# Optimization experiments

Measured on AMD Instinct MI355X. Metric: run time of the kernel, lower is better.

Reference implementation:

```python
import jax, jax.numpy as jnp
import numpy as np

N_IMG, C_IN, H, W = 8, 8, 136, 200
N_INST = 512
CHANNELS = 8
STRIDE = 8
MASK_OUT_STRIDE = 4
# sizes_of_interest + [last*2], per __init__
SOI = jnp.asarray([64.0, 128.0, 256.0, 512.0, 1024.0, 2048.0], dtype=jnp.float32)
W_NUMS = [(C_IN + 2) * CHANNELS, CHANNELS * CHANNELS, CHANNELS]
B_NUMS = [CHANNELS, CHANNELS, 1]
N_PARAMS = sum(W_NUMS) + sum(B_NUMS)  # 169


def compute_locations(h, w, stride):
    # matches adet compute_locations: centers of stride-sized cells, (x, y)
    shifts_x = jnp.arange(w, dtype=jnp.float32) * stride + stride // 2
    shifts_y = jnp.arange(h, dtype=jnp.float32) * stride + stride // 2
    ys, xs = jnp.meshgrid(shifts_y, shifts_x, indexing='ij')
    return jnp.stack([xs.reshape(-1), ys.reshape(-1)], axis=1)  # [h*w, 2]


def bilinear_up_align_corners(x, out_h, out_w):
    # x: [n, h, w]; F.interpolate(mode='bilinear', align_corners=True)
    n, h, w = x.shape
    ys = jnp.linspace(0.0, h - 1.0, out_h)
    xs = jnp.linspace(0.0, w - 1.0, out_w)
    y0 = jnp.floor(ys).astype(jnp.int32)
    x0 = jnp.floor(xs).astype(jnp.int32)
    y1 = jnp.minimum(y0 + 1, h - 1)
    x1 = jnp.minimum(x0 + 1, w - 1)
    wy = (ys - y0.astype(jnp.float32))[None, :, None]
    wx = (xs - x0.astype(jnp.float32))[None, None, :]
    top = x[:, y0, :]
    bot = x[:, y1, :]
    row0 = top[:, :, x0] * (1.0 - wx) + top[:, :, x1] * wx
    row1 = bot[:, :, x0] * (1.0 - wx) + bot[:, :, x1] * wx
    return row0 * (1.0 - wy) + row1 * wy


def dice_coefficient(x, target):
    eps = 1e-5
    n = x.shape[0]
    x = x.reshape(n, -1)
    target = target.reshape(n, -1)
    intersection = jnp.sum(x * target, axis=1)
    union = jnp.sum(x * x, axis=1) + jnp.sum(target * target, axis=1) + eps
    return 1.0 - 2.0 * intersection / union


def setup_inputs() -> dict:
    key = jax.random.key(0)
    ks = jax.random.split(key, 6)
    mask_feats = jax.random.normal(ks[0], (N_IMG, C_IN, H, W), jnp.float32)
    mask_head_params = jax.random.normal(ks[1], (N_INST, N_PARAMS), jnp.float32) * 0.1
    instance_locations = jax.random.uniform(ks[2], (N_INST, 2), jnp.float32) * jnp.asarray(
        [W * STRIDE, H * STRIDE], dtype=jnp.float32)
    gt_masks = (jax.random.uniform(ks[3], (N_INST, 2 * H, 2 * W), jnp.float32) > 0.5).astype(jnp.float32)
    im_inds = jax.random.randint(ks[4], (N_INST,), 0, N_IMG, jnp.int32)
    fpn_levels = jax.random.randint(ks[5], (N_INST,), 0, 5, jnp.int32)
    return {
        'mask_feats': mask_feats,
        'mask_head_params': mask_head_params,
        'instance_locations': instance_locations,
        'gt_masks': gt_masks,
        'im_inds': im_inds,
        'fpn_levels': fpn_levels,
        'mask_feat_stride': 8,
    }


def reference(mask_feats, mask_head_params, instance_locations, gt_masks, im_inds, fpn_levels, mask_feat_stride):
    n_inst = mask_head_params.shape[0]
    # relative coordinates: instance center minus every grid location, / size-of-interest
    locations = compute_locations(H, W, mask_feat_stride)          # [H*W, 2]
    rel = instance_locations[:, None, :] - locations[None, :, :]   # [n, H*W, 2]
    rel = jnp.transpose(rel, (0, 2, 1)) / SOI[fpn_levels][:, None, None]
    rel = rel.reshape(n_inst, 2, H, W)
    feats = mask_feats[im_inds]                                    # gather [n, C_IN, H, W]
    x = jnp.concatenate([rel, feats], axis=1)                      # [n, C_IN+2, H, W]

    # parse_dynamic_params: split per-instance params into 1x1 conv weights/biases
    splits = np.cumsum(W_NUMS + B_NUMS)[:-1].tolist()
    p = jnp.split(mask_head_params, splits, axis=1)
    w0 = p[0].reshape(n_inst, CHANNELS, C_IN + 2)
    w1 = p[1].reshape(n_inst, CHANNELS, CHANNELS)
    w2 = p[2].reshape(n_inst, 1, CHANNELS)
    b0, b1, b2 = p[3], p[4], p[5]

    # grouped 1x1 convs (groups = n_inst) == per-instance channel GEMM
    x = jax.nn.relu(jnp.einsum('nchw,noc->nohw', x, w0) + b0[:, :, None, None])
    x = jax.nn.relu(jnp.einsum('nchw,noc->nohw', x, w1) + b1[:, :, None, None])
    logits = jnp.einsum('nchw,noc->nohw', x, w2) + b2[:, :, None, None]  # [n, 1, H, W]

    up = mask_feat_stride // MASK_OUT_STRIDE
    logits_up = bilinear_up_align_corners(logits[:, 0], H * up, W * up)
    scores = jax.nn.sigmoid(logits_up)
    loss = dice_coefficient(scores, gt_masks)                      # [n]
    return loss
```

## Files before the change

### kernel.cpp

```cpp
#include <hip/hip_runtime.h>
#include <math.h>

#define NIMG 8
#define CIN 8
#define Hh 136
#define Ww 200
#define HW (Hh * Ww)
#define OH 272
#define OW 400
#define NINST 512
#define NPAR 169
#define TROWS 34
#define NTILES 8
#define LROWS 19
#define PART_BYTES ((size_t)NINST * NTILES * 3 * 4)

#define PINV(x) asm volatile("" : "+v"(x))
#define PINS(x) asm volatile("" : "+s"(x))
#define MEMFENCE asm volatile("" ::: "memory")
#define SCHEDBAR __builtin_amdgcn_sched_barrier(0)

__device__ __forceinline__ void mlp_tile_reg(
    float* __restrict__ slog, const float* __restrict__ fb0,
    const float* __restrict__ pp, int ly0, int lycnt, int tid,
    const float (&A0)[8], const float (&Ax)[8], const float (&Ay)[8])
{
    const int tpx = lycnt * Ww;
    const float* fbase = fb0 + ly0 * Ww;

    for (int px = tid * 2; px < tpx; px += 512) {
        MEMFENCE;
        float Wf[64];
#pragma unroll
        for (int o = 0; o < 8; o++)
#pragma unroll
            for (int c = 0; c < 8; c++) Wf[o * 8 + c] = pp[o * 10 + 2 + c];
#pragma unroll
        for (int i = 0; i < 64; i++) PINS(Wf[i]);

        const int yy = px / 200;
        const int x  = px - yy * 200;
        const float yf = (float)(ly0 + yy);
        const float* fb = fbase + px;
        float f[8][2];
#pragma unroll
        for (int c = 0; c < 8; c++) {
            const float2 t = *reinterpret_cast<const float2*>(fb + c * HW);
            f[c][0] = t.x; f[c][1] = t.y;
        }
        float h[8][2];
#pragma unroll
        for (int o = 0; o < 8; o++) {
            const float pre = A0[o] + Ay[o] * yf;
#pragma unroll
            for (int p = 0; p < 2; p++) {
                const float xf = (float)(x + p);
                float a = pre + Ax[o] * xf;
#pragma unroll
                for (int c = 0; c < 8; c++) a += Wf[o * 8 + c] * f[c][p];
                h[o][p] = fmaxf(a, 0.0f);
            }
        }
#pragma unroll
        for (int o = 0; o < 8; o++) { PINV(h[o][0]); PINV(h[o][1]); }
        SCHEDBAR;

        MEMFENCE;
        float w1[64];
#pragma unroll
        for (int k = 0; k < 64; k++) w1[k] = pp[80 + k];
#pragma unroll
        for (int k = 0; k < 64; k++) PINS(w1[k]);
        float w2[8], b1[8], b2;
#pragma unroll
        for (int k = 0; k < 8; k++) { w2[k] = pp[144 + k]; b1[k] = pp[160 + k]; }
        b2 = pp[168];
#pragma unroll
        for (int k = 0; k < 8; k++) { PINV(w2[k]); PINV(b1[k]); }
        PINV(b2);

        float o2[2];
#pragma unroll
        for (int p = 0; p < 2; p++) {
            float g[8];
#pragma unroll
            for (int o = 0; o < 8; o++) {
                float a = b1[o];
#pragma unroll
                for (int c = 0; c < 8; c++) a += w1[o * 8 + c] * h[c][p];
                g[o] = fmaxf(a, 0.0f);
            }
            float lg = b2;
#pragma unroll
            for (int c = 0; c < 8; c++) lg += w2[c] * g[c];
            o2[p] = lg;
        }
        *reinterpret_cast<float2*>(&slog[px]) = make_float2(o2[0], o2[1]);
        SCHEDBAR;
    }
}

__device__ __forceinline__ void dice_tile(
    const float* __restrict__ slog, const float* __restrict__ gtn,
    int oy0, int ly0, int lycnt, int tid,
    float& aI, float& aS, float& aT)
{
    const float sy = 135.0f / 271.0f;
    const float sx = 199.0f / 399.0f;
    for (int g4 = tid; g4 < TROWS * (OW / 4); g4 += 256) {
        const int ry = g4 / 100;
        const int gx = (g4 - ry * 100) * 4;
        const int oy = oy0 + ry;
        const float ysf = (float)oy * sy;
        const int y0 = (int)ysf;
        const float wy = ysf - (float)y0;
        const int y1 = (y0 + 1 > Hh - 1) ? (Hh - 1) : (y0 + 1);
        int r0i = y0 - ly0, r1i = y1 - ly0;
        r0i = r0i < 0 ? 0 : (r0i > lycnt - 1 ? lycnt - 1 : r0i);
        r1i = r1i < 0 ? 0 : (r1i > lycnt - 1 ? lycnt - 1 : r1i);
        const float* s0 = &slog[r0i * Ww];
        const float* s1 = &slog[r1i * Ww];

        const float4 t4 = *reinterpret_cast<const float4*>(gtn + ry * OW + gx);
        const float tv[4] = { t4.x, t4.y, t4.z, t4.w };
#pragma unroll
        for (int p = 0; p < 4; p++) {
            const int ox = gx + p;
            const float xsf = (float)ox * sx;
            const int x0 = (int)xsf;
            const float wx = xsf - (float)x0;
            const int x1 = (x0 + 1 > Ww - 1) ? (Ww - 1) : (x0 + 1);
            const float v00 = s0[x0];
            const float v01 = s0[x1];
            const float v10 = s1[x0];
            const float v11 = s1[x1];
            const float top = v00 + wx * (v01 - v00);
            const float bot = v10 + wx * (v11 - v10);
            const float v   = top + wy * (bot - top);
            const float s   = __fdividef(1.0f, 1.0f + __expf(-v));
            aI += s * tv[p];
            aS += s * s;
            aT += tv[p];
        }
    }
}

#define LOAD_AFFINE                                                             \
    const float ix = iloc[2 * n + 0];                                           \
    const float iy = iloc[2 * n + 1];                                           \
    const int   im = iminds[n];                                                 \
    const float invsoi = 1.0f / (float)(64 << lvls[n]);                         \
    const float* pp = pars + n * NPAR;                                          \
    float A0[8], Ax[8], Ay[8];                                                  \
    _Pragma("unroll")                                                           \
    for (int o = 0; o < 8; o++) {                                               \
        const float wx0 = pp[o * 10 + 0];                                       \
        const float wy0 = pp[o * 10 + 1];                                       \
        Ax[o] = -8.0f * invsoi * wx0;                                           \
        Ay[o] = -8.0f * invsoi * wy0;                                           \
        A0[o] = pp[152 + o] + (wx0 * (ix - 4.0f) + wy0 * (iy - 4.0f)) * invsoi; \
    }                                                                           \
    _Pragma("unroll")                                                           \
    for (int o = 0; o < 8; o++) { PINV(A0[o]); PINV(Ax[o]); PINV(Ay[o]); }

__global__ __launch_bounds__(256, 6) void dmh_tile(
    const float* __restrict__ feats,
    const float* __restrict__ pars,
    const float* __restrict__ iloc,
    const float* __restrict__ gt,
    const int* __restrict__ iminds,
    const int* __restrict__ lvls,
    float* __restrict__ part)
{
    __shared__ float slog[LROWS * Ww];
    __shared__ float sred[12];

    const int n    = blockIdx.y;
    const int tile = blockIdx.x;
    const int tid  = threadIdx.x;

    LOAD_AFFINE

    const float sy = 135.0f / 271.0f;
    const int oy0 = tile * TROWS;
    const int ly0 = (int)((float)oy0 * sy);
    int lyL = (int)((float)(oy0 + TROWS - 1) * sy) + 1;
    if (lyL > Hh - 1) lyL = Hh - 1;
    const int lycnt = lyL - ly0 + 1;

    const float* fb0 = feats + (size_t)im * (CIN * HW);
    mlp_tile_reg(slog, fb0, pp, ly0, lycnt, tid, A0, Ax, Ay);
    __syncthreads();

    float aI = 0.0f, aS = 0.0f, aT = 0.0f;
    const float* gtn = gt + (size_t)n * (OH * OW) + (size_t)oy0 * OW;
    dice_tile(slog, gtn, oy0, ly0, lycnt, tid, aI, aS, aT);

#pragma unroll
    for (int off = 32; off > 0; off >>= 1) {
        aI += __shfl_down(aI, off, 64);
        aS += __shfl_down(aS, off, 64);
        aT += __shfl_down(aT, off, 64);
    }
    const int wv = tid >> 6;
    if ((tid & 63) == 0) {
        sred[wv * 3 + 0] = aI;
        sred[wv * 3 + 1] = aS;
        sred[wv * 3 + 2] = aT;
    }
    __syncthreads();
    if (tid == 0) {
        float* pt = part + (size_t)(n * NTILES + tile) * 3;
        pt[0] = sred[0] + sred[3] + sred[6] + sred[9];
        pt[1] = sred[1] + sred[4] + sred[7] + sred[10];
        pt[2] = sred[2] + sred[5] + sred[8] + sred[11];
    }
}

__global__ __launch_bounds__(256) void dmh_fin2(const float* __restrict__ part,
                                                float* __restrict__ out)
{
    const int i = blockIdx.x * 256 + threadIdx.x;
    if (i < NINST) {
        float I = 0.0f, S = 0.0f, T = 0.0f;
#pragma unroll
        for (int t = 0; t < NTILES; t++) {
            const float* pt = part + (size_t)(i * NTILES + t) * 3;
            I += pt[0]; S += pt[1]; T += pt[2];
        }
        out[i] = 1.0f - 2.0f * I / (S + T + 1e-5f);
    }
}

__global__ __launch_bounds__(256, 6) void dmh_one(
    const float* __restrict__ feats,
    const float* __restrict__ pars,
    const float* __restrict__ iloc,
    const float* __restrict__ gt,
    const int* __restrict__ iminds,
    const int* __restrict__ lvls,
    float* __restrict__ out)
{
    __shared__ float slog[LROWS * Ww];
    __shared__ float sred[12];

    const int n   = blockIdx.x;
    const int tid = threadIdx.x;

    LOAD_AFFINE

    const float sy = 135.0f / 271.0f;
    const float* fb0 = feats + (size_t)im * (CIN * HW);

    float aI = 0.0f, aS = 0.0f, aT = 0.0f;
    for (int tile = 0; tile < NTILES; tile++) {
        const int oy0 = tile * TROWS;
        const int ly0 = (int)((float)oy0 * sy);
        int lyL = (int)((float)(oy0 + TROWS - 1) * sy) + 1;
        if (lyL > Hh - 1) lyL = Hh - 1;
        const int lycnt = lyL - ly0 + 1;

        mlp_tile_reg(slog, fb0, pp, ly0, lycnt, tid, A0, Ax, Ay);
        __syncthreads();
        const float* gtn = gt + (size_t)n * (OH * OW) + (size_t)oy0 * OW;
        dice_tile(slog, gtn, oy0, ly0, lycnt, tid, aI, aS, aT);
        __syncthreads();
    }

#pragma unroll
    for (int off = 32; off > 0; off >>= 1) {
        aI += __shfl_down(aI, off, 64);
        aS += __shfl_down(aS, off, 64);
        aT += __shfl_down(aT, off, 64);
    }
    const int wv = tid >> 6;
    if ((tid & 63) == 0) {
        sred[wv * 3 + 0] = aI;
        sred[wv * 3 + 1] = aS;
        sred[wv * 3 + 2] = aT;
    }
    __syncthreads();
    if (tid == 0) {
        const float I = sred[0] + sred[3] + sred[6] + sred[9];
        const float S = sred[1] + sred[4] + sred[7] + sred[10];
        const float T = sred[2] + sred[5] + sred[8] + sred[11];
        out[n] = 1.0f - 2.0f * I / (S + T + 1e-5f);
    }
}

extern "C" void kernel_launch(void* const* d_in, const int* in_sizes, int n_in,
                              void* d_out, int out_size, void* d_ws, size_t ws_size,
                              hipStream_t stream) {
    const float* feats  = (const float*)d_in[0];
    const float* pars   = (const float*)d_in[1];
    const float* iloc   = (const float*)d_in[2];
    const float* gt     = (const float*)d_in[3];
    const int*   iminds = (const int*)d_in[4];
    const int*   lvls   = (const int*)d_in[5];

    if (ws_size >= PART_BYTES) {
        float* part = (float*)d_ws;
        dim3 g(NTILES, NINST);
        dmh_tile<<<g, 256, 0, stream>>>(feats, pars, iloc, gt, iminds, lvls, part);
        dmh_fin2<<<(NINST + 255) / 256, 256, 0, stream>>>(part, (float*)d_out);
    } else {
        dmh_one<<<NINST, 256, 0, stream>>>(feats, pars, iloc, gt, iminds, lvls,
                                           (float*)d_out);
    }
}
```

Before: 394.6 us.

## Warp-specialize MLP into layer0 producer and layer1/2 consumer via double-buffered LDS

The tile kernel now splits its 256 threads into two groups. Threads 0-127 load features and compute the first 1x1 conv layer into a double-buffered shared strip of hidden activations, while threads 128-255 apply the second and third layers to the previous strip. The goal is to overlap global feature loads with the later layers and keep each group's weights in registers without reloading them every iteration. The cost is extra shared memory (32 KB) and a barrier per strip, and the occupancy hint drops from 6 to 3 blocks.

```diff
diff --git a/kernel.cpp b/kernel.cpp
--- a/kernel.cpp
+++ b/kernel.cpp
@@ -13,92 +13,13 @@
 #define TROWS 34
 #define NTILES 8
 #define LROWS 19
+#define SPX 512
 #define PART_BYTES ((size_t)NINST * NTILES * 3 * 4)
 
 #define PINV(x) asm volatile("" : "+v"(x))
 #define PINS(x) asm volatile("" : "+s"(x))
 #define MEMFENCE asm volatile("" ::: "memory")
 #define SCHEDBAR __builtin_amdgcn_sched_barrier(0)
-
-__device__ __forceinline__ void mlp_tile_reg(
-    float* __restrict__ slog, const float* __restrict__ fb0,
-    const float* __restrict__ pp, int ly0, int lycnt, int tid,
-    const float (&A0)[8], const float (&Ax)[8], const float (&Ay)[8])
-{
-    const int tpx = lycnt * Ww;
-    const float* fbase = fb0 + ly0 * Ww;
-
-    for (int px = tid * 2; px < tpx; px += 512) {
-        MEMFENCE;
-        float Wf[64];
-#pragma unroll
-        for (int o = 0; o < 8; o++)
-#pragma unroll
-            for (int c = 0; c < 8; c++) Wf[o * 8 + c] = pp[o * 10 + 2 + c];
-#pragma unroll
-        for (int i = 0; i < 64; i++) PINS(Wf[i]);
-
-        const int yy = px / 200;
-        const int x  = px - yy * 200;
-        const float yf = (float)(ly0 + yy);
-        const float* fb = fbase + px;
-        float f[8][2];
-#pragma unroll
-        for (int c = 0; c < 8; c++) {
-            const float2 t = *reinterpret_cast<const float2*>(fb + c * HW);
-            f[c][0] = t.x; f[c][1] = t.y;
-        }
-        float h[8][2];
-#pragma unroll
-        for (int o = 0; o < 8; o++) {
-            const float pre = A0[o] + Ay[o] * yf;
-#pragma unroll
-            for (int p = 0; p < 2; p++) {
-                const float xf = (float)(x + p);
-                float a = pre + Ax[o] * xf;
-#pragma unroll
-                for (int c = 0; c < 8; c++) a += Wf[o * 8 + c] * f[c][p];
-                h[o][p] = fmaxf(a, 0.0f);
-            }
-        }
-#pragma unroll
-        for (int o = 0; o < 8; o++) { PINV(h[o][0]); PINV(h[o][1]); }
-        SCHEDBAR;
-
-        MEMFENCE;
-        float w1[64];
-#pragma unroll
-        for (int k = 0; k < 64; k++) w1[k] = pp[80 + k];
-#pragma unroll
-        for (int k = 0; k < 64; k++) PINS(w1[k]);
-        float w2[8], b1[8], b2;
-#pragma unroll
-        for (int k = 0; k < 8; k++) { w2[k] = pp[144 + k]; b1[k] = pp[160 + k]; }
-        b2 = pp[168];
-#pragma unroll
-        for (int k = 0; k < 8; k++) { PINV(w2[k]); PINV(b1[k]); }
-        PINV(b2);
-
-        float o2[2];
-#pragma unroll
-        for (int p = 0; p < 2; p++) {
-            float g[8];
-#pragma unroll
-            for (int o = 0; o < 8; o++) {
-                float a = b1[o];
-#pragma unroll
-                for (int c = 0; c < 8; c++) a += w1[o * 8 + c] * h[c][p];
-                g[o] = fmaxf(a, 0.0f);
-            }
-            float lg = b2;
-#pragma unroll
-            for (int c = 0; c < 8; c++) lg += w2[c] * g[c];
-            o2[p] = lg;
-        }
-        *reinterpret_cast<float2*>(&slog[px]) = make_float2(o2[0], o2[1]);
-        SCHEDBAR;
-    }
-}
 
 __device__ __forceinline__ void dice_tile(
     const float* __restrict__ slog, const float* __restrict__ gtn,
@@ -145,25 +66,7 @@
     }
 }
 
-#define LOAD_AFFINE                                                             \
-    const float ix = iloc[2 * n + 0];                                           \
-    const float iy = iloc[2 * n + 1];                                           \
-    const int   im = iminds[n];                                                 \
-    const float invsoi = 1.0f / (float)(64 << lvls[n]);                         \
-    const float* pp = pars + n * NPAR;                                          \
-    float A0[8], Ax[8], Ay[8];                                                  \
-    _Pragma("unroll")                                                           \
-    for (int o = 0; o < 8; o++) {                                               \
-        const float wx0 = pp[o * 10 + 0];                                       \
-        const float wy0 = pp[o * 10 + 1];                                       \
-        Ax[o] = -8.0f * invsoi * wx0;                                           \
-        Ay[o] = -8.0f * invsoi * wy0;                                           \
-        A0[o] = pp[152 + o] + (wx0 * (ix - 4.0f) + wy0 * (iy - 4.0f)) * invsoi; \
-    }                                                                           \
-    _Pragma("unroll")                                                           \
-    for (int o = 0; o < 8; o++) { PINV(A0[o]); PINV(Ax[o]); PINV(Ay[o]); }
-
-__global__ __launch_bounds__(256, 6) void dmh_tile(
+__global__ __launch_bounds__(256, 3) void dmh_tile(
     const float* __restrict__ feats,
     const float* __restrict__ pars,
     const float* __restrict__ iloc,
@@ -173,13 +76,12 @@
     float* __restrict__ part)
 {
     __shared__ float slog[LROWS * Ww];
+    __shared__ float hbuf[2][8][SPX];
     __shared__ float sred[12];
 
     const int n    = blockIdx.y;
     const int tile = blockIdx.x;
     const int tid  = threadIdx.x;
-
-    LOAD_AFFINE
 
     const float sy = 135.0f / 271.0f;
     const int oy0 = tile * TROWS;
@@ -187,10 +89,120 @@
     int lyL = (int)((float)(oy0 + TROWS - 1) * sy) + 1;
     if (lyL > Hh - 1) lyL = Hh - 1;
     const int lycnt = lyL - ly0 + 1;
-
-    const float* fb0 = feats + (size_t)im * (CIN * HW);
-    mlp_tile_reg(slog, fb0, pp, ly0, lycnt, tid, A0, Ax, Ay);
-    __syncthreads();
+    const int tpx = lycnt * Ww;
+    const int nstrips = (tpx + SPX - 1) / SPX;
+
+    const float* pp = pars + n * NPAR;
+
+    if (tid < 128) {
+        const float ix = iloc[2 * n + 0];
+        const float iy = iloc[2 * n + 1];
+        const int   im = iminds[n];
+        const float invsoi = 1.0f / (float)(64 << lvls[n]);
+        float Wf[64], A0[8], Ax[8], Ay[8];
+#pragma unroll
+        for (int o = 0; o < 8; o++) {
+            const float wx0 = pp[o * 10 + 0];
+            const float wy0 = pp[o * 10 + 1];
+            Ax[o] = -8.0f * invsoi * wx0;
+            Ay[o] = -8.0f * invsoi * wy0;
+            A0[o] = pp[152 + o] + (wx0 * (ix - 4.0f) + wy0 * (iy - 4.0f)) * invsoi;
+#pragma unroll
+            for (int c = 0; c < 8; c++) Wf[o * 8 + c] = pp[o * 10 + 2 + c];
+        }
+#pragma unroll
+        for (int i = 0; i < 64; i++) PINS(Wf[i]);
+#pragma unroll
+        for (int o = 0; o < 8; o++) { PINV(A0[o]); PINV(Ax[o]); PINV(Ay[o]); }
+
+        const float* fbase = feats + (size_t)im * (CIN * HW) + ly0 * Ww;
+
+        for (int k = 0; k < nstrips + 1; ++k) {
+            if (k < nstrips) {
+                const int base = k * SPX + tid * 4;
+                if (base < tpx) {
+                    const int yy = base / 200;
+                    const int x  = base - yy * 200;
+                    const float yf = (float)(ly0 + yy);
+                    const float* fb = fbase + base;
+                    float f[8][4];
+#pragma unroll
+                    for (int c = 0; c < 8; c++) {
+                        const float4 t = *reinterpret_cast<const float4*>(fb + c * HW);
+                        f[c][0] = t.x; f[c][1] = t.y; f[c][2] = t.z; f[c][3] = t.w;
+                    }
+#pragma unroll
+                    for (int o = 0; o < 8; o++) {
+                        const float pre = A0[o] + Ay[o] * yf;
+                        float hv[4];
+#pragma unroll
+                        for (int p = 0; p < 4; p++) {
+                            const float xf = (float)(x + p);
+                            float a = pre + Ax[o] * xf;
+#pragma unroll
+                            for (int c = 0; c < 8; c++) a += Wf[o * 8 + c] * f[c][p];
+                            hv[p] = fmaxf(a, 0.0f);
+                        }
+                        *reinterpret_cast<float4*>(&hbuf[k & 1][o][tid * 4]) =
+                            make_float4(hv[0], hv[1], hv[2], hv[3]);
+                    }
+                }
+            }
+            __syncthreads();
+        }
+    } else {
+        float w1[64], w2[8], b1[8], b2;
+#pragma unroll
+        for (int k = 0; k < 64; k++) w1[k] = pp[80 + k];
+#pragma unroll
+        for (int k = 0; k < 8; k++) { w2[k] = pp[144 + k]; b1[k] = pp[160 + k]; }
+        b2 = pp[168];
+#pragma unroll
+        for (int k = 0; k < 64; k++) PINV(w1[k]);
+#pragma unroll
+        for (int k = 0; k < 8; k++) { PINV(w2[k]); PINV(b1[k]); }
+        PINV(b2);
+
+        const int ct = tid - 128;
+
+        for (int k = 0; k < nstrips + 1; ++k) {
+            if (k >= 1) {
+                const int km = k - 1;
+                const int base = km * SPX + ct * 4;
+                if (base < tpx) {
+                    float o4[4];
+#pragma unroll
+                    for (int half = 0; half < 2; half++) {
+                        float h[8][2];
+#pragma unroll
+                        for (int c = 0; c < 8; c++) {
+                            const float2 t = *reinterpret_cast<const float2*>(
+                                &hbuf[km & 1][c][ct * 4 + half * 2]);
+                            h[c][0] = t.x; h[c][1] = t.y;
+                        }
+#pragma unroll
+                        for (int p = 0; p < 2; p++) {
+                            float g[8];
+#pragma unroll
+                            for (int o = 0; o < 8; o++) {
+                                float a = b1[o];
+#pragma unroll
+                                for (int c = 0; c < 8; c++) a += w1[o * 8 + c] * h[c][p];
+                                g[o] = fmaxf(a, 0.0f);
+                            }
+                            float lg = b2;
+#pragma unroll
+                            for (int c = 0; c < 8; c++) lg += w2[c] * g[c];
+                            o4[half * 2 + p] = lg;
+                        }
+                    }
+                    *reinterpret_cast<float4*>(&slog[base]) =
+                        make_float4(o4[0], o4[1], o4[2], o4[3]);
+                }
+            }
+            __syncthreads();
+        }
+    }
 
     float aI = 0.0f, aS = 0.0f, aT = 0.0f;
     const float* gtn = gt + (size_t)n * (OH * OW) + (size_t)oy0 * OW;
@@ -232,7 +244,87 @@
     }
 }
 
-__global__ __launch_bounds__(256, 6) void dmh_one(
+__device__ __forceinline__ void mlp_tile_reg(
+    float* __restrict__ slog, const float* __restrict__ fb0,
+    const float* __restrict__ pp, int ly0, int lycnt, int tid,
+    const float (&A0)[8], const float (&Ax)[8], const float (&Ay)[8])
+{
+    const int tpx = lycnt * Ww;
+    const float* fbase = fb0 + ly0 * Ww;
+
+    for (int px = tid * 2; px < tpx; px += 512) {
+        MEMFENCE;
+        float Wf[64];
+#pragma unroll
+        for (int o = 0; o < 8; o++)
+#pragma unroll
+            for (int c = 0; c < 8; c++) Wf[o * 8 + c] = pp[o * 10 + 2 + c];
+#pragma unroll
+        for (int i = 0; i < 64; i++) PINS(Wf[i]);
+
+        const int yy = px / 200;
+        const int x  = px - yy * 200;
+        const float yf = (float)(ly0 + yy);
+        const float* fb = fbase + px;
+        float f[8][2];
+#pragma unroll
+        for (int c = 0; c < 8; c++) {
+            const float2 t = *reinterpret_cast<const float2*>(fb + c * HW);
+            f[c][0] = t.x; f[c][1] = t.y;
+        }
+        float h[8][2];
+#pragma unroll
+        for (int o = 0; o < 8; o++) {
+            const float pre = A0[o] + Ay[o] * yf;
+#pragma unroll
+            for (int p = 0; p < 2; p++) {
+                const float xf = (float)(x + p);
+                float a = pre + Ax[o] * xf;
+#pragma unroll
+                for (int c = 0; c < 8; c++) a += Wf[o * 8 + c] * f[c][p];
+                h[o][p] = fmaxf(a, 0.0f);
+            }
+        }
+#pragma unroll
+        for (int o = 0; o < 8; o++) { PINV(h[o][0]); PINV(h[o][1]); }
+        SCHEDBAR;
+
+        MEMFENCE;
+        float w1[64];
+#pragma unroll
+        for (int k = 0; k < 64; k++) w1[k] = pp[80 + k];
+#pragma unroll
+        for (int k = 0; k < 64; k++) PINS(w1[k]);
+        float w2[8], b1[8], b2;
+#pragma unroll
+        for (int k = 0; k < 8; k++) { w2[k] = pp[144 + k]; b1[k] = pp[160 + k]; }
+        b2 = pp[168];
+#pragma unroll
+        for (int k = 0; k < 8; k++) { PINV(w2[k]); PINV(b1[k]); }
+        PINV(b2);
+
+        float o2[2];
+#pragma unroll
+        for (int p = 0; p < 2; p++) {
+            float g[8];
+#pragma unroll
+            for (int o = 0; o < 8; o++) {
+                float a = b1[o];
+#pragma unroll
+                for (int c = 0; c < 8; c++) a += w1[o * 8 + c] * h[c][p];
+                g[o] = fmaxf(a, 0.0f);
+            }
+            float lg = b2;
+#pragma unroll
+            for (int c = 0; c < 8; c++) lg += w2[c] * g[c];
+            o2[p] = lg;
+        }
+        *reinterpret_cast<float2*>(&slog[px]) = make_float2(o2[0], o2[1]);
+        SCHEDBAR;
+    }
+}
+
+__global__ __launch_bounds__(256, 3) void dmh_one(
     const float* __restrict__ feats,
     const float* __restrict__ pars,
     const float* __restrict__ iloc,
@@ -247,7 +339,22 @@
     const int n   = blockIdx.x;
     const int tid = threadIdx.x;
 
-    LOAD_AFFINE
+    const float ix = iloc[2 * n + 0];
+    const float iy = iloc[2 * n + 1];
+    const int   im = iminds[n];
+    const float invsoi = 1.0f / (float)(64 << lvls[n]);
+    const float* pp = pars + n * NPAR;
+    float A0[8], Ax[8], Ay[8];
+#pragma unroll
+    for (int o = 0; o < 8; o++) {
+        const float wx0 = pp[o * 10 + 0];
+        const float wy0 = pp[o * 10 + 1];
+        Ax[o] = -8.0f * invsoi * wx0;
+        Ay[o] = -8.0f * invsoi * wy0;
+        A0[o] = pp[152 + o] + (wx0 * (ix - 4.0f) + wy0 * (iy - 4.0f)) * invsoi;
+    }
+#pragma unroll
+    for (int o = 0; o < 8; o++) { PINV(A0[o]); PINV(Ax[o]); PINV(Ay[o]); }
 
     const float sy = 135.0f / 271.0f;
     const float* fb0 = feats + (size_t)im * (CIN * HW);
```

Result: slower. 403.8 us (+2.3%).
